# Performance work log

Measured on AMD Instinct MI355X. Metric: run time of the kernel, lower is better.

## Reference

```python
import jax, jax.numpy as jnp
import numpy as np

B, T, D, V, CD, NF = 2, 2048, 1024, 32000, 1024, 4
EPS_NORM = 1e-12
EPS_LN = 1e-5


def _gelu(x):
    return jax.nn.gelu(x, approximate=False)


def _l2norm(x):
    n = jnp.linalg.norm(x, axis=-1, keepdims=True)
    return x / jnp.maximum(n, EPS_NORM)


def setup_inputs() -> dict:
    key = jax.random.key(0)
    ks = jax.random.split(key, 24)
    s = 0.02
    inp = {
        "tokens": jax.random.randint(ks[0], (B, T), 0, V),
        "c_states": jax.random.normal(ks[1], (8, CD), dtype=jnp.float32),
        "embed": jax.random.normal(ks[2], (V, D), dtype=jnp.float32) * s,
        "pos_embed": jax.random.normal(ks[3], (T, D), dtype=jnp.float32) * s,
        # c_to_topo: Linear(c_dim,64) -> GELU -> Linear(64,2) -> Softplus (dead code in fwd, kept for completeness)
        "topo_W1": jax.random.normal(ks[4], (CD, 64), dtype=jnp.float32) * s,
        "topo_b1": jnp.zeros((64,), jnp.float32),
        "topo_W2": jax.random.normal(ks[5], (64, 2), dtype=jnp.float32) * s,
        "topo_b2": jnp.zeros((2,), jnp.float32),
        # c_to_thresh: Linear(c_dim,32) -> GELU -> Linear(32,NF) -> Sigmoid
        "thr_W1": jax.random.normal(ks[6], (CD, 32), dtype=jnp.float32) * s,
        "thr_b1": jnp.zeros((32,), jnp.float32),
        "thr_W2": jax.random.normal(ks[7], (32, NF), dtype=jnp.float32) * s,
        "thr_b2": jnp.zeros((NF,), jnp.float32),
        # simplex layers: NF x (Linear(2D,D) -> GELU -> Linear(D,D))
        "simp_W1": jax.random.normal(ks[8], (NF, 2 * D, D), dtype=jnp.float32) * s,
        "simp_b1": jnp.zeros((NF, D), jnp.float32),
        "simp_W2": jax.random.normal(ks[9], (NF, D, D), dtype=jnp.float32) * s,
        "simp_b2": jnp.zeros((NF, D), jnp.float32),
        # topo_integrate: Linear(D+2, 2D) -> GELU -> Linear(2D, D)
        "int_W1": jax.random.normal(ks[10], (D + 2, 2 * D), dtype=jnp.float32) * s,
        "int_b1": jnp.zeros((2 * D,), jnp.float32),
        "int_W2": jax.random.normal(ks[11], (2 * D, D), dtype=jnp.float32) * s,
        "int_b2": jnp.zeros((D,), jnp.float32),
        "ln_g": jnp.ones((D,), jnp.float32),
        "ln_b": jnp.zeros((D,), jnp.float32),
        "head_W": jax.random.normal(ks[12], (D, V), dtype=jnp.float32) * s,
    }
    return inp


def _forward(tokens, c_states, embed, pos_embed,
             topo_W1, topo_b1, topo_W2, topo_b2,
             thr_W1, thr_b1, thr_W2, thr_b2,
             simp_W1, simp_b1, simp_W2, simp_b2,
             int_W1, int_b1, int_W2, int_b2,
             ln_g, ln_b, head_W):
    b, t = tokens.shape
    x = embed[tokens] + pos_embed[jnp.arange(t)][None]          # [B,T,D]
    c_pooled = c_states.mean(axis=0)                            # [CD]
    thresholds = jax.nn.sigmoid(_gelu(c_pooled @ thr_W1 + thr_b1) @ thr_W2 + thr_b2)  # [NF]

    for level in range(NF):
        thresh = thresholds[level]
        x0 = x[0]                                               # [T,D] (module only uses batch elem 0)
        xn = _l2norm(x0)
        sim = xn @ xn.T                                         # [T,T]
        adj = jax.nn.sigmoid(10.0 * (sim - thresh))
        agg = adj @ x0                                          # dense message aggregation
        combined = jnp.concatenate([x0, agg], axis=-1)          # [T,2D]
        update = _gelu(combined @ simp_W1[level] + simp_b1[level]) @ simp_W2[level] + simp_b2[level]
        x = x + update[None] * 0.2                              # broadcast update across batch

    # approximate Betti numbers on detached embeddings
    xd = jax.lax.stop_gradient(x[0])
    xn = _l2norm(xd)
    sim = xn @ xn.T
    adj = jax.nn.sigmoid(10.0 * (sim - 0.5))
    degree = adj.sum(axis=-1)
    beta0 = (degree < 0.5).astype(jnp.float32).sum()
    n_edges = adj.sum() / 2.0
    beta1 = jax.nn.relu(n_edges - jnp.float32(t) + beta0 + 1.0)
    betti = jnp.stack([beta0, beta1])                           # [2]
    betti_exp = jnp.broadcast_to(betti[None, None, :], (b, t, 2))

    x = jnp.concatenate([x, betti_exp], axis=-1)                # [B,T,D+2]
    x = _gelu(x @ int_W1 + int_b1) @ int_W2 + int_b2            # [B,T,D]
    mu = x.mean(axis=-1, keepdims=True)
    var = x.var(axis=-1, keepdims=True)
    x = (x - mu) / jnp.sqrt(var + EPS_LN) * ln_g + ln_b
    return x @ head_W                                           # [B,T,V]


def reference(tokens, c_states, embed, pos_embed,
              topo_W1, topo_b1, topo_W2, topo_b2,
              thr_W1, thr_b1, thr_W2, thr_b2,
              simp_W1, simp_b1, simp_W2, simp_b2,
              int_W1, int_b1, int_W2, int_b2,
              ln_g, ln_b, head_W):
    return _forward(tokens, c_states, embed, pos_embed,
                    topo_W1, topo_b1, topo_W2, topo_b2,
                    thr_W1, thr_b1, thr_W2, thr_b2,
                    simp_W1, simp_b1, simp_W2, simp_b2,
                    int_W1, int_b1, int_W2, int_b2,
                    ln_g, ln_b, head_W)
```

## Files before the change

### kernel.cpp

```cpp
#include <hip/hip_runtime.h>

typedef __bf16 bf16;
using bf16x8 = __attribute__((ext_vector_type(8))) __bf16;
using bf16x4 = __attribute__((ext_vector_type(4))) __bf16;
using f32x4  = __attribute__((ext_vector_type(4))) float;

#define DEV __device__ __forceinline__
#define SCHED_FENCE() __builtin_amdgcn_sched_barrier(0)

DEV float gelu_f(float x){ return 0.5f*x*(1.0f+erff(x*0.7071067811865475f)); }
DEV float sigm_f(float x){ return 1.0f/(1.0f+expf(-x)); }

DEV void gload16(const bf16* g, bf16* l){
    __builtin_amdgcn_global_load_lds(
        (const __attribute__((address_space(1))) void*)g,
        (__attribute__((address_space(3))) void*)l, 16, 0, 0);
}

enum { EPI_ADJ=0, EPI_BF16=1, EPI_GELU_BIAS=2, EPI_XUPD=3, EPI_BIAS_F32=4, EPI_F32=5 };

template<int BM,int BN,int WM,int WN,int MINW,int EPI>
__global__ __launch_bounds__(WM*WN*64, MINW)
void gemm_p(const bf16* __restrict__ A, const bf16* __restrict__ B,
            int M, int N, int K, void* __restrict__ Cout, int ldc,
            const float* __restrict__ bias, const float* __restrict__ scal, int sidx,
            float* __restrict__ xu0, float* __restrict__ xu1)
{
    constexpr int THREADS = WM*WN*64;
    constexpr int MR = BM/WM/16, NR = BN/WN/16;
    constexpr int ATILE = BM*64, BTILE = BN*64;
    constexpr int RR = THREADS/8;
    constexpr int VM = (BM+BN)/RR;
    __shared__ bf16 sm[2*(ATILE+BTILE)];

    const int nbm = M/BM, nbn = N/BN;
    const int nwg = nbm*nbn;
    int wg = blockIdx.x;
    wg = (wg&7)*(nwg>>3) + (wg>>3);
    const int by = wg % nbm, bx = wg / nbm;
    const int tid = threadIdx.x, lane = tid&63, wid = tid>>6;
    const int wm = wid / WN, wn = wid % WN;
    const int fr = lane&15, fq = lane>>4;

    const bf16* Ab = A + (long)(by*BM + (tid>>3))*K + (((tid&7) ^ ((tid>>3)&7))<<3);
    const bf16* Bb = B + (long)(bx*BN + (tid>>3))*K + (((tid&7) ^ ((tid>>3)&7))<<3);

    auto STAGE = [&](int tt, int cb){
        bf16* d = sm + cb*(ATILE+BTILE) + wid*512;
        const long ko = (long)tt*64;
#pragma unroll
        for (int g=0; g<BM/RR; ++g)
            gload16(Ab + (long)g*RR*K + ko, d + g*RR*64);
#pragma unroll
        for (int g=0; g<BN/RR; ++g)
            gload16(Bb + (long)g*RR*K + ko, d + ATILE + g*RR*64);
    };

    f32x4 acc[MR][NR] = {};
    const int nt = K >> 6;

    STAGE(0,0);
    STAGE(1,1);

    for (int t=0; t<nt; ++t){
        const bf16* bufA = sm + (t&1)*(ATILE+BTILE);
        const bf16* bufB = bufA + ATILE;
        if (t+1<nt){
            if constexpr (VM==6)      asm volatile("s_waitcnt vmcnt(6)" ::: "memory");
            else if constexpr (VM==8) asm volatile("s_waitcnt vmcnt(8)" ::: "memory");
            else                      asm volatile("s_waitcnt vmcnt(0)" ::: "memory");
        } else {
            asm volatile("s_waitcnt vmcnt(0)" ::: "memory");
        }
        __builtin_amdgcn_s_barrier();
        __builtin_amdgcn_sched_barrier(0);
#pragma unroll
        for (int ks=0; ks<2; ++ks){
            bf16x8 af[MR], bv[NR];
            const int ch = (((ks*4+fq) ^ (fr&7))<<3);
#pragma unroll
            for (int j=0;j<MR;++j)
                af[j] = *(const bf16x8*)&bufA[(wm*(MR*16) + j*16 + fr)*64 + ch];
#pragma unroll
            for (int j=0;j<NR;++j)
                bv[j] = *(const bf16x8*)&bufB[(wn*(NR*16) + j*16 + fr)*64 + ch];
            __builtin_amdgcn_s_setprio(1);
#pragma unroll
            for (int mi=0;mi<MR;++mi)
#pragma unroll
            for (int ni=0;ni<NR;++ni)
                acc[mi][ni] = __builtin_amdgcn_mfma_f32_16x16x32_bf16(
                    af[mi], bv[ni], acc[mi][ni], 0,0,0);
            __builtin_amdgcn_s_setprio(0);
        }
        asm volatile("s_waitcnt lgkmcnt(0)" ::: "memory");
        __builtin_amdgcn_s_barrier();
        if (t+2<nt) STAGE(t+2, t&1);
    }

    float thr = 0.f;
    if constexpr (EPI==EPI_ADJ) thr = scal[sidx];

#pragma unroll
    for (int mi=0;mi<MR;++mi){
#pragma unroll
        for (int ni=0;ni<NR;++ni){
            const int col = bx*BN + wn*(NR*16) + ni*16 + fr;
#pragma unroll
            for (int r=0;r<4;++r){
                const int row = by*BM + wm*(MR*16) + mi*16 + fq*4 + r;
                const float v = acc[mi][ni][r];
                const long ci = (long)row*ldc + col;
                if constexpr (EPI==EPI_ADJ)       ((bf16*)Cout)[ci] = (bf16)sigm_f(10.f*(v - thr));
                else if constexpr (EPI==EPI_BF16) ((bf16*)Cout)[ci] = (bf16)v;
                else if constexpr (EPI==EPI_GELU_BIAS) ((bf16*)Cout)[ci] = (bf16)gelu_f(v + bias[col]);
                else if constexpr (EPI==EPI_BIAS_F32)  ((float*)Cout)[ci] = v + bias[col];
                else if constexpr (EPI==EPI_F32)       ((float*)Cout)[ci] = v;
                else if constexpr (EPI==EPI_XUPD){
                    const float u = 0.2f*(v + bias[col]);
                    xu0[ci] += u;  xu1[ci] += u;
                }
            }
        }
    }
}

template<int EPI>
__global__ __launch_bounds__(512, 2)
void gemm8(const bf16* __restrict__ A, const bf16* __restrict__ B,
           int M, int N, int K, void* __restrict__ Cout, int ldc,
           const float* __restrict__ bias)
{
    __shared__ bf16 sm[65536];
    const int nbm = M>>8, nbn = N>>8;
    const int nwg = nbm*nbn;
    int wg = blockIdx.x;
    wg = (wg&7)*(nwg>>3) + (wg>>3);
    const int bx = wg % nbn, by = wg / nbn;
    const int tid = threadIdx.x, lane = tid&63, wid = tid>>6;
    const int wm = wid>>2, wn = wid&3;
    const int fr = lane&15, fq = lane>>4;

    const bf16* Ag = A + (long)(by*256 + (tid>>3))*K + (((tid&7) ^ ((tid>>3)&7))<<3);
    const bf16* Bg = B + (long)(bx*256 + (tid>>3))*K + (((tid&7) ^ ((tid>>3)&7))<<3);

    auto SA = [&](int tt, int h){
        bf16* d = sm + (tt&1)*32768 + wid*512;
        const long ko = (long)tt*64;
        gload16(Ag + (long)(h*64)*K + ko,       d + h*4096);
        gload16(Ag + (long)(128+h*64)*K + ko,   d + 8192 + h*4096);
    };
    auto SB = [&](int tt, int h){
        bf16* d = sm + (tt&1)*32768 + 16384 + wid*512;
        const long ko = (long)tt*64;
#pragma unroll
        for (int g=0; g<2; ++g)
            gload16(Bg + (long)(h*2+g)*64*K + ko, d + (h*2+g)*4096);
    };

    f32x4 acc[8][4] = {};
    bf16x8 aCur[8], b0[4], b1[4];
    const int nt = K >> 6;

    SA(0,0); SB(0,0); SA(0,1); SB(0,1);
    SA(1,0); SB(1,0); SA(1,1);
    SCHED_FENCE();

    for (int t=0; t<nt; ++t){
        const bf16* bufA = sm + (t&1)*32768;
        const bf16* bufB = bufA + 16384;

        auto LDA = [&](int mh){
#pragma unroll
            for (int ks=0;ks<2;++ks){
                const int ch = (((ks*4+fq) ^ (fr&7))<<3);
#pragma unroll
                for (int j=0;j<4;++j)
                    aCur[ks*4+j] = *(const bf16x8*)&bufA[(wm*128 + mh*64 + j*16 + fr)*64 + ch];
            }
        };
        auto LDB = [&](int nh, bf16x8* dst){
#pragma unroll
            for (int ks=0;ks<2;++ks){
                const int ch = (((ks*4+fq) ^ (fr&7))<<3);
#pragma unroll
                for (int j=0;j<2;++j)
                    dst[ks*2+j] = *(const bf16x8*)&bufB[(wn*64 + nh*32 + j*16 + fr)*64 + ch];
            }
        };
        auto QMFMA = [&](int mh, int nh, bf16x8* bArr){
            __builtin_amdgcn_s_setprio(1);
#pragma unroll
            for (int ks=0;ks<2;++ks)
#pragma unroll
            for (int j=0;j<4;++j)
#pragma unroll
            for (int jj=0;jj<2;++jj)
                acc[mh*4+j][nh*2+jj] = __builtin_amdgcn_mfma_f32_16x16x32_bf16(
                    aCur[ks*4+j], bArr[ks*2+jj], acc[mh*4+j][nh*2+jj], 0,0,0);
            __builtin_amdgcn_s_setprio(0);
            SCHED_FENCE();
        };

        if (t+1<nt) asm volatile("s_waitcnt vmcnt(6)" ::: "memory");
        else        asm volatile("s_waitcnt vmcnt(0)" ::: "memory");
        __builtin_amdgcn_s_barrier();
        SCHED_FENCE();
        if (t+1<nt) SB(t+1,1);
        SCHED_FENCE();
        LDA(0); LDB(0, b0);
        asm volatile("s_waitcnt lgkmcnt(0)" ::: "memory");
        SCHED_FENCE();
        QMFMA(0,0,b0);
        __builtin_amdgcn_s_barrier();
        SCHED_FENCE();
        if (t+2<nt) SA(t+2,0);
        SCHED_FENCE();
        LDB(1, b1);
        asm volatile("s_waitcnt lgkmcnt(0)" ::: "memory");
        SCHED_FENCE();
        QMFMA(0,1,b1);
        __builtin_amdgcn_s_barrier();
        SCHED_FENCE();
        if (t+2<nt) SB(t+2,0);
        SCHED_FENCE();
        LDA(1);
        asm volatile("s_waitcnt lgkmcnt(0)" ::: "memory");
        SCHED_FENCE();
        QMFMA(1,1,b1);
        __builtin_amdgcn_s_barrier();
        SCHED_FENCE();
        if (t+2<nt) SA(t+2,1);
        SCHED_FENCE();
        QMFMA(1,0,b0);
    }

#pragma unroll
    for (int mi=0;mi<8;++mi){
#pragma unroll
        for (int ni=0;ni<4;++ni){
            const int col = bx*256 + wn*64 + ni*16 + fr;
#pragma unroll
            for (int r=0;r<4;++r){
                const int row = by*256 + wm*128 + mi*16 + fq*4 + r;
                const float v = acc[mi][ni][r];
                const long ci = (long)row*ldc + col;
                if constexpr (EPI==EPI_F32)            ((float*)Cout)[ci] = v;
                else if constexpr (EPI==EPI_BIAS_F32)  ((float*)Cout)[ci] = v + bias[col];
                else                                   ((bf16*)Cout)[ci] = (bf16)v;
            }
        }
    }
}

__global__ void prep_kernel(const float* __restrict__ cs,
                            const float* __restrict__ W1, const float* __restrict__ b1,
                            const float* __restrict__ W2, const float* __restrict__ b2,
                            float* __restrict__ thrs)
{
    __shared__ float cp[1024];
    __shared__ float part[8][32];
    __shared__ float h[32];
    const int tid = threadIdx.x;
    for (int j = tid; j < 1024; j += 256){
        float s = 0.f;
#pragma unroll
        for (int r = 0; r < 8; r++) s += cs[r*1024 + j];
        cp[j] = s * 0.125f;
    }
    __syncthreads();
    const int t = tid & 31, g = tid >> 5;
    float p = 0.f;
    for (int j = g*128; j < g*128+128; j++) p += cp[j] * W1[j*32 + t];
    part[g][t] = p;
    __syncthreads();
    if (tid < 32){
        float s = b1[tid];
#pragma unroll
        for (int q=0;q<8;q++) s += part[q][tid];
        h[tid] = gelu_f(s);
    }
    __syncthreads();
    if (tid < 4){
        float z = b2[tid];
        for (int k=0;k<32;k++) z += h[k]*W2[k*4 + tid];
        thrs[tid] = sigm_f(z);
    }
    if (tid == 4) thrs[4] = 0.5f;
}

__global__ void embed_kernel(const int* __restrict__ tok, const float* __restrict__ emb,
                             const float* __restrict__ pos, float* __restrict__ x)
{
    const long i = (long)blockIdx.x*256 + threadIdx.x;
    const int  d4 = i & 255;
    const long bt = i >> 8;
    const int  t  = (int)(bt & 2047);
    const int  token = tok[bt];
    f32x4 e = *(const f32x4*)(emb + (long)token*1024 + d4*4);
    f32x4 p = *(const f32x4*)(pos + (long)t*1024 + d4*4);
    *(f32x4*)(x + i*4) = e + p;
}

__global__ void transpose_f2b(const float* __restrict__ in, int ldin, long istr,
                              bf16* __restrict__ out, int ldout, long ostr,
                              int R, int C)
{
    __shared__ float tile[32][33];
    const int nbx = C >> 5, nby = R >> 5;
    const int per = nbx*nby;
    const int l  = blockIdx.x / per;
    const int rm = blockIdx.x % per;
    const int bx = rm % nbx, by = rm / nbx;
    const float* inl = in + (long)l*istr;
    bf16* outl = out + (long)l*ostr;
    const int tx = threadIdx.x & 31, ty = threadIdx.x >> 5;
#pragma unroll
    for (int i=0;i<32;i+=8)
        tile[ty+i][tx] = inl[(long)(by*32+ty+i)*ldin + bx*32+tx];
    __syncthreads();
#pragma unroll
    for (int i=0;i<32;i+=8)
        outl[(long)(bx*32+ty+i)*ldout + by*32+tx] = (bf16)tile[tx][ty+i];
}

__global__ void rownorm_kernel(const float* __restrict__ x, bf16* __restrict__ xn,
                               bf16* __restrict__ x0b, int ld0)
{
    const long t = blockIdx.x; const int tid = threadIdx.x;
    f32x4 v = *(const f32x4*)(x + t*1024 + tid*4);
    float s = v.x*v.x + v.y*v.y + v.z*v.z + v.w*v.w;
#pragma unroll
    for (int o=32;o>0;o>>=1) s += __shfl_down(s, o);
    __shared__ float red[4];
    if ((tid&63)==0) red[tid>>6] = s;
    __syncthreads();
    const float tot = red[0]+red[1]+red[2]+red[3];
    const float inv = 1.0f / fmaxf(sqrtf(tot), 1e-12f);
    bf16x4 a, b;
    a[0]=(bf16)(v.x*inv); a[1]=(bf16)(v.y*inv); a[2]=(bf16)(v.z*inv); a[3]=(bf16)(v.w*inv);
    b[0]=(bf16)v.x; b[1]=(bf16)v.y; b[2]=(bf16)v.z; b[3]=(bf16)v.w;
    *(bf16x4*)(xn  + t*1024 + tid*4) = a;
    *(bf16x4*)(x0b + t*ld0  + tid*4) = b;
}

__global__ void degree_kernel(const bf16* __restrict__ adj, float* __restrict__ deg)
{
    const long t = blockIdx.x; const int tid = threadIdx.x;
    bf16x8 v = *(const bf16x8*)(adj + t*2048 + tid*8);
    float s = 0.f;
#pragma unroll
    for (int j=0;j<8;j++) s += (float)v[j];
#pragma unroll
    for (int o=32;o>0;o>>=1) s += __shfl_down(s, o);
    __shared__ float red[4];
    if ((tid&63)==0) red[tid>>6] = s;
    __syncthreads();
    if (tid==0) deg[t] = red[0]+red[1]+red[2]+red[3];
}

__global__ void betti_kernel(const float* __restrict__ deg, float* __restrict__ betti)
{
    const int tid = threadIdx.x;
    float s = 0.f, c = 0.f;
#pragma unroll
    for (int i=0;i<8;i++){
        const float d = deg[tid*8 + i];
        s += d;  c += (d < 0.5f) ? 1.f : 0.f;
    }
#pragma unroll
    for (int o=32;o>0;o>>=1){ s += __shfl_down(s,o); c += __shfl_down(c,o); }
    __shared__ float ss[4], cc[4];
    if ((tid&63)==0){ ss[tid>>6]=s; cc[tid>>6]=c; }
    __syncthreads();
    if (tid==0){
        const float S = ss[0]+ss[1]+ss[2]+ss[3];
        const float C = cc[0]+cc[1]+cc[2]+cc[3];
        const float ne = 0.5f*S;
        const float b1 = ne - 2048.f + C + 1.f;
        betti[0] = C;
        betti[1] = b1 > 0.f ? b1 : 0.f;
    }
}

__global__ void b1eff_kernel(const float* __restrict__ ib1, const float* __restrict__ iW1,
                             const float* __restrict__ betti, float* __restrict__ out)
{
    const int j = blockIdx.x*256 + threadIdx.x;
    out[j] = ib1[j] + betti[0]*iW1[(long)1024*2048 + j] + betti[1]*iW1[(long)1025*2048 + j];
}

__global__ void f2b_kernel(const float* __restrict__ in, bf16* __restrict__ out)
{
    const long i = (long)blockIdx.x*256 + threadIdx.x;
    f32x4 a = *(const f32x4*)(in + i*8);
    f32x4 c = *(const f32x4*)(in + i*8 + 4);
    bf16x8 o;
    o[0]=(bf16)a.x; o[1]=(bf16)a.y; o[2]=(bf16)a.z; o[3]=(bf16)a.w;
    o[4]=(bf16)c.x; o[5]=(bf16)c.y; o[6]=(bf16)c.z; o[7]=(bf16)c.w;
    *(bf16x8*)(out + i*8) = o;
}

__global__ void ln_kernel(const float* __restrict__ y, const float* __restrict__ g,
                          const float* __restrict__ b, bf16* __restrict__ out)
{
    const long t = blockIdx.x; const int tid = threadIdx.x;
    f32x4 v = *(const f32x4*)(y + t*1024 + tid*4);
    float s  = v.x+v.y+v.z+v.w;
    float s2 = v.x*v.x+v.y*v.y+v.z*v.z+v.w*v.w;
#pragma unroll
    for (int o=32;o>0;o>>=1){ s += __shfl_down(s,o); s2 += __shfl_down(s2,o); }
    __shared__ float ss[4], qq[4];
    if ((tid&63)==0){ ss[tid>>6]=s; qq[tid>>6]=s2; }
    __syncthreads();
    const float S = ss[0]+ss[1]+ss[2]+ss[3], Q = qq[0]+qq[1]+qq[2]+qq[3];
    const float mu  = S * (1.f/1024.f);
    const float var = Q * (1.f/1024.f) - mu*mu;
    const float inv = rsqrtf(var + 1e-5f);
    f32x4 gv = *(const f32x4*)(g + tid*4);
    f32x4 bv = *(const f32x4*)(b + tid*4);
    bf16x4 o;
    o[0] = (bf16)((v.x - mu)*inv*gv.x + bv.x);
    o[1] = (bf16)((v.y - mu)*inv*gv.y + bv.y);
    o[2] = (bf16)((v.z - mu)*inv*gv.z + bv.z);
    o[3] = (bf16)((v.w - mu)*inv*gv.w + bv.w);
    *(bf16x4*)(out + t*1024 + tid*4) = o;
}

extern "C" void kernel_launch(void* const* d_in, const int* in_sizes, int n_in,
                              void* d_out, int out_size, void* d_ws, size_t ws_size,
                              hipStream_t stream)
{
    const int*   tokens = (const int*)  d_in[0];
    const float* cstate = (const float*)d_in[1];
    const float* embedW = (const float*)d_in[2];
    const float* posW   = (const float*)d_in[3];
    const float* thrW1  = (const float*)d_in[8];
    const float* thrb1  = (const float*)d_in[9];
    const float* thrW2  = (const float*)d_in[10];
    const float* thrb2  = (const float*)d_in[11];
    const float* simpW1 = (const float*)d_in[12];
    const float* simpb1 = (const float*)d_in[13];
    const float* simpW2 = (const float*)d_in[14];
    const float* simpb2 = (const float*)d_in[15];
    const float* intW1  = (const float*)d_in[16];
    const float* intb1  = (const float*)d_in[17];
    const float* intW2  = (const float*)d_in[18];
    const float* intb2  = (const float*)d_in[19];
    const float* lng    = (const float*)d_in[20];
    const float* lnb    = (const float*)d_in[21];
    const float* headW  = (const float*)d_in[22];
    float* out = (float*)d_out;

    size_t off = 0;
    auto carve = [&](size_t bytes) -> void* {
        void* p = (char*)d_ws + off;
        off += (bytes + 255) & ~(size_t)255;
        return p;
    };
    float* x_f32   = (float*)carve(16777216);
    bf16*  xn      = (bf16*) carve(4194304);
    bf16*  x0T     = (bf16*) carve(4194304);
    bf16*  comb    = (bf16*) carve(8388608);
    bf16*  adj     = (bf16*) carve(8388608);
    bf16*  h1      = (bf16*) carve(4194304);
    bf16*  xb      = (bf16*) carve(8388608);
    bf16*  w1T     = (bf16*) carve(16777216);
    bf16*  w2T     = (bf16*) carve(8388608);
    bf16*  i1T     = (bf16*) carve(4194304);
    bf16*  i2T     = (bf16*) carve(4194304);
    bf16*  hT      = (bf16*) carve(65536000);
    float* degree  = (float*)carve(8192);
    float* b1eff   = (float*)carve(8192);
    float* thrs    = (float*)carve(64);
    float* betti   = (float*)carve(64);
    bf16*  h2  = comb;
    float* yv  = x_f32;
    bf16*  xln = xn;

    const dim3 blk(256);
    const dim3 blk512(512);

    prep_kernel<<<1, blk, 0, stream>>>(cstate, thrW1, thrb1, thrW2, thrb2, thrs);
    embed_kernel<<<4096, blk, 0, stream>>>(tokens, embedW, posW, x_f32);

    transpose_f2b<<<4*(1024/32)*(2048/32), blk, 0, stream>>>(
        simpW1, 1024, (long)2048*1024, w1T, 2048, (long)1024*2048, 2048, 1024);
    transpose_f2b<<<4*(1024/32)*(1024/32), blk, 0, stream>>>(
        simpW2, 1024, (long)1024*1024, w2T, 1024, (long)1024*1024, 1024, 1024);
    transpose_f2b<<<(2048/32)*(1024/32), blk, 0, stream>>>(
        intW1, 2048, 0, i1T, 1024, 0, 1024, 2048);
    transpose_f2b<<<(1024/32)*(2048/32), blk, 0, stream>>>(
        intW2, 1024, 0, i2T, 2048, 0, 2048, 1024);
    transpose_f2b<<<(32000/32)*(1024/32), blk, 0, stream>>>(
        headW, 32000, 0, hT, 1024, 0, 1024, 32000);

    for (int l=0;l<4;l++){
        rownorm_kernel<<<2048, blk, 0, stream>>>(x_f32, xn, comb, 2048);
        transpose_f2b<<<(1024/32)*(2048/32), blk, 0, stream>>>(
            x_f32, 1024, 0, x0T, 2048, 0, 2048, 1024);
        gemm_p<128,128,2,2,2,EPI_ADJ><<<16*16, blk, 0, stream>>>(
            xn, xn, 2048, 2048, 1024, adj, 2048, nullptr, thrs, l, nullptr, nullptr);
        gemm_p<64,128,2,2,3,EPI_BF16><<<32*8, blk, 0, stream>>>(
            adj, x0T, 2048, 1024, 2048, comb + 1024, 2048, nullptr, nullptr, 0, nullptr, nullptr);
        gemm_p<64,128,2,2,3,EPI_GELU_BIAS><<<32*8, blk, 0, stream>>>(
            comb, w1T + (long)l*1024*2048, 2048, 1024, 2048, h1, 1024,
            simpb1 + l*1024, nullptr, 0, nullptr, nullptr);
        gemm_p<64,128,2,2,3,EPI_XUPD><<<32*8, blk, 0, stream>>>(
            h1, w2T + (long)l*1024*1024, 2048, 1024, 1024, nullptr, 1024,
            simpb2 + l*1024, nullptr, 0, x_f32, x_f32 + (long)2048*1024);
    }

    rownorm_kernel<<<2048, blk, 0, stream>>>(x_f32, xn, comb, 2048);
    gemm_p<128,128,2,2,2,EPI_ADJ><<<16*16, blk, 0, stream>>>(
        xn, xn, 2048, 2048, 1024, adj, 2048, nullptr, thrs, 4, nullptr, nullptr);
    degree_kernel<<<2048, blk, 0, stream>>>(adj, degree);
    betti_kernel<<<1, blk, 0, stream>>>(degree, betti);
    b1eff_kernel<<<8, blk, 0, stream>>>(intb1, intW1, betti, b1eff);

    f2b_kernel<<<2048, blk, 0, stream>>>(x_f32, xb);
    gemm_p<128,128,2,2,2,EPI_GELU_BIAS><<<32*16, blk, 0, stream>>>(
        xb, i1T, 4096, 2048, 1024, h2, 2048, b1eff, nullptr, 0, nullptr, nullptr);
    gemm_p<128,128,2,2,2,EPI_BIAS_F32><<<32*8, blk, 0, stream>>>(
        h2, i2T, 4096, 1024, 2048, yv, 1024, intb2, nullptr, 0, nullptr, nullptr);
    ln_kernel<<<4096, blk, 0, stream>>>(yv, lng, lnb, xln);
    gemm8<EPI_F32><<<16*125, blk512, 0, stream>>>(
        xln, hT, 4096, 32000, 1024, out, 32000, nullptr);
}
```

Baseline: 862.1 us.

## Compute symmetric adjacency upper triangle only and mirror; fuse bf16 cast into update

The Gram-matrix adjacency GEMM now launches only upper-triangular 128x128 tiles (136 instead of 256) and a new mirror kernel copies them across the diagonal, relying on the adjacency being symmetric. The last simplex update epilogue writes a bf16 copy of x directly, which removes the separate f2b conversion kernel. The final rownorm also skips its unused bf16 copy. Together these halve adjacency GEMM work and save several memory passes, at the cost of an extra transpose-style pass over half of adj and a serial tile-index loop. The 136 triangular tiles may also fill the GPU less evenly than 256 did.

```diff
diff --git a/kernel.cpp b/kernel.cpp
--- a/kernel.cpp
+++ b/kernel.cpp
@@ -17,14 +17,14 @@
         (__attribute__((address_space(3))) void*)l, 16, 0, 0);
 }
 
-enum { EPI_ADJ=0, EPI_BF16=1, EPI_GELU_BIAS=2, EPI_XUPD=3, EPI_BIAS_F32=4, EPI_F32=5 };
-
-template<int BM,int BN,int WM,int WN,int MINW,int EPI>
+enum { EPI_ADJ=0, EPI_BF16=1, EPI_GELU_BIAS=2, EPI_XUPD=3, EPI_BIAS_F32=4, EPI_F32=5, EPI_XUPDB=6 };
+
+template<int BM,int BN,int WM,int WN,int MINW,int TRIU,int EPI>
 __global__ __launch_bounds__(WM*WN*64, MINW)
 void gemm_p(const bf16* __restrict__ A, const bf16* __restrict__ B,
             int M, int N, int K, void* __restrict__ Cout, int ldc,
             const float* __restrict__ bias, const float* __restrict__ scal, int sidx,
-            float* __restrict__ xu0, float* __restrict__ xu1)
+            float* __restrict__ xu0, float* __restrict__ xu1, bf16* __restrict__ xbp)
 {
     constexpr int THREADS = WM*WN*64;
     constexpr int MR = BM/WM/16, NR = BN/WN/16;
@@ -34,10 +34,17 @@
     __shared__ bf16 sm[2*(ATILE+BTILE)];
 
     const int nbm = M/BM, nbn = N/BN;
-    const int nwg = nbm*nbn;
+    const int nwg = TRIU ? (nbm*(nbm+1))/2 : nbm*nbn;
     int wg = blockIdx.x;
     wg = (wg&7)*(nwg>>3) + (wg>>3);
-    const int by = wg % nbm, bx = wg / nbm;
+    int by, bx;
+    if constexpr (TRIU){
+        int i = wg, r = 0;
+        while (i >= nbm - r){ i -= nbm - r; ++r; }
+        by = r; bx = r + i;
+    } else {
+        by = wg % nbm; bx = wg / nbm;
+    }
     const int tid = threadIdx.x, lane = tid&63, wid = tid>>6;
     const int wm = wid / WN, wn = wid % WN;
     const int fr = lane&15, fq = lane>>4;
@@ -120,9 +127,35 @@
                     const float u = 0.2f*(v + bias[col]);
                     xu0[ci] += u;  xu1[ci] += u;
                 }
+                else if constexpr (EPI==EPI_XUPDB){
+                    const float u = 0.2f*(v + bias[col]);
+                    const float n0 = xu0[ci] + u, n1 = xu1[ci] + u;
+                    xu0[ci] = n0;  xu1[ci] = n1;
+                    xbp[ci] = (bf16)n0;
+                    xbp[ci + (long)2048*1024] = (bf16)n1;
+                }
             }
         }
     }
+}
+
+__global__ void mirror_kernel(bf16* __restrict__ adj)
+{
+    const int b = blockIdx.x;
+    int t128 = b >> 4, sub = b & 15;
+    int i = t128, BY = 1;
+    while (i >= BY){ i -= BY; ++BY; }
+    const int BX = i;
+    const int r0 = BY*128 + (sub>>2)*32, c0 = BX*128 + (sub&3)*32;
+    __shared__ bf16 tile[32][33];
+    const int tx = threadIdx.x & 31, ty = threadIdx.x >> 5;
+#pragma unroll
+    for (int k=0;k<32;k+=8)
+        tile[ty+k][tx] = adj[(long)(c0+ty+k)*2048 + r0+tx];
+    __syncthreads();
+#pragma unroll
+    for (int k=0;k<32;k+=8)
+        adj[(long)(r0+ty+k)*2048 + c0+tx] = tile[tx][ty+k];
 }
 
 template<int EPI>
@@ -337,11 +370,14 @@
     __syncthreads();
     const float tot = red[0]+red[1]+red[2]+red[3];
     const float inv = 1.0f / fmaxf(sqrtf(tot), 1e-12f);
-    bf16x4 a, b;
+    bf16x4 a;
     a[0]=(bf16)(v.x*inv); a[1]=(bf16)(v.y*inv); a[2]=(bf16)(v.z*inv); a[3]=(bf16)(v.w*inv);
-    b[0]=(bf16)v.x; b[1]=(bf16)v.y; b[2]=(bf16)v.z; b[3]=(bf16)v.w;
-    *(bf16x4*)(xn  + t*1024 + tid*4) = a;
-    *(bf16x4*)(x0b + t*ld0  + tid*4) = b;
+    *(bf16x4*)(xn + t*1024 + tid*4) = a;
+    if (x0b){
+        bf16x4 b;
+        b[0]=(bf16)v.x; b[1]=(bf16)v.y; b[2]=(bf16)v.z; b[3]=(bf16)v.w;
+        *(bf16x4*)(x0b + t*ld0 + tid*4) = b;
+    }
 }
 
 __global__ void degree_kernel(const bf16* __restrict__ adj, float* __restrict__ deg)
@@ -388,17 +424,6 @@
 {
     const int j = blockIdx.x*256 + threadIdx.x;
     out[j] = ib1[j] + betti[0]*iW1[(long)1024*2048 + j] + betti[1]*iW1[(long)1025*2048 + j];
-}
-
-__global__ void f2b_kernel(const float* __restrict__ in, bf16* __restrict__ out)
-{
-    const long i = (long)blockIdx.x*256 + threadIdx.x;
-    f32x4 a = *(const f32x4*)(in + i*8);
-    f32x4 c = *(const f32x4*)(in + i*8 + 4);
-    bf16x8 o;
-    o[0]=(bf16)a.x; o[1]=(bf16)a.y; o[2]=(bf16)a.z; o[3]=(bf16)a.w;
-    o[4]=(bf16)c.x; o[5]=(bf16)c.y; o[6]=(bf16)c.z; o[7]=(bf16)c.w;
-    *(bf16x8*)(out + i*8) = o;
 }
 
 __global__ void ln_kernel(const float* __restrict__ y, const float* __restrict__ g,
@@ -499,30 +524,36 @@
         rownorm_kernel<<<2048, blk, 0, stream>>>(x_f32, xn, comb, 2048);
         transpose_f2b<<<(1024/32)*(2048/32), blk, 0, stream>>>(
             x_f32, 1024, 0, x0T, 2048, 0, 2048, 1024);
-        gemm_p<128,128,2,2,2,EPI_ADJ><<<16*16, blk, 0, stream>>>(
-            xn, xn, 2048, 2048, 1024, adj, 2048, nullptr, thrs, l, nullptr, nullptr);
-        gemm_p<64,128,2,2,3,EPI_BF16><<<32*8, blk, 0, stream>>>(
-            adj, x0T, 2048, 1024, 2048, comb + 1024, 2048, nullptr, nullptr, 0, nullptr, nullptr);
-        gemm_p<64,128,2,2,3,EPI_GELU_BIAS><<<32*8, blk, 0, stream>>>(
+        gemm_p<128,128,2,2,2,1,EPI_ADJ><<<136, blk, 0, stream>>>(
+            xn, xn, 2048, 2048, 1024, adj, 2048, nullptr, thrs, l, nullptr, nullptr, nullptr);
+        mirror_kernel<<<1920, blk, 0, stream>>>(adj);
+        gemm_p<64,128,2,2,3,0,EPI_BF16><<<32*8, blk, 0, stream>>>(
+            adj, x0T, 2048, 1024, 2048, comb + 1024, 2048, nullptr, nullptr, 0, nullptr, nullptr, nullptr);
+        gemm_p<64,128,2,2,3,0,EPI_GELU_BIAS><<<32*8, blk, 0, stream>>>(
             comb, w1T + (long)l*1024*2048, 2048, 1024, 2048, h1, 1024,
-            simpb1 + l*1024, nullptr, 0, nullptr, nullptr);
-        gemm_p<64,128,2,2,3,EPI_XUPD><<<32*8, blk, 0, stream>>>(
-            h1, w2T + (long)l*1024*1024, 2048, 1024, 1024, nullptr, 1024,
-            simpb2 + l*1024, nullptr, 0, x_f32, x_f32 + (long)2048*1024);
-    }
-
-    rownorm_kernel<<<2048, blk, 0, stream>>>(x_f32, xn, comb, 2048);
-    gemm_p<128,128,2,2,2,EPI_ADJ><<<16*16, blk, 0, stream>>>(
-        xn, xn, 2048, 2048, 1024, adj, 2048, nullptr, thrs, 4, nullptr, nullptr);
+            simpb1 + l*1024, nullptr, 0, nullptr, nullptr, nullptr);
+        if (l < 3)
+            gemm_p<64,128,2,2,3,0,EPI_XUPD><<<32*8, blk, 0, stream>>>(
+                h1, w2T + (long)l*1024*1024, 2048, 1024, 1024, nullptr, 1024,
+                simpb2 + l*1024, nullptr, 0, x_f32, x_f32 + (long)2048*1024, nullptr);
+        else
+            gemm_p<64,128,2,2,3,0,EPI_XUPDB><<<32*8, blk, 0, stream>>>(
+                h1, w2T + (long)l*1024*1024, 2048, 1024, 1024, nullptr, 1024,
+                simpb2 + l*1024, nullptr, 0, x_f32, x_f32 + (long)2048*1024, xb);
+    }
+
+    rownorm_kernel<<<2048, blk, 0, stream>>>(x_f32, xn, nullptr, 0);
+    gemm_p<128,128,2,2,2,1,EPI_ADJ><<<136, blk, 0, stream>>>(
+        xn, xn, 2048, 2048, 1024, adj, 2048, nullptr, thrs, 4, nullptr, nullptr, nullptr);
+    mirror_kernel<<<1920, blk, 0, stream>>>(adj);
     degree_kernel<<<2048, blk, 0, stream>>>(adj, degree);
     betti_kernel<<<1, blk, 0, stream>>>(degree, betti);
     b1eff_kernel<<<8, blk, 0, stream>>>(intb1, intW1, betti, b1eff);
 
-    f2b_kernel<<<2048, blk, 0, stream>>>(x_f32, xb);
-    gemm_p<128,128,2,2,2,EPI_GELU_BIAS><<<32*16, blk, 0, stream>>>(
-        xb, i1T, 4096, 2048, 1024, h2, 2048, b1eff, nullptr, 0, nullptr, nullptr);
-    gemm_p<128,128,2,2,2,EPI_BIAS_F32><<<32*8, blk, 0, stream>>>(
-        h2, i2T, 4096, 1024, 2048, yv, 1024, intb2, nullptr, 0, nullptr, nullptr);
+    gemm_p<128,128,2,2,2,0,EPI_GELU_BIAS><<<32*16, blk, 0, stream>>>(
+        xb, i1T, 4096, 2048, 1024, h2, 2048, b1eff, nullptr, 0, nullptr, nullptr, nullptr);
+    gemm_p<128,128,2,2,2,0,EPI_BIAS_F32><<<32*8, blk, 0, stream>>>(
+        h2, i2T, 4096, 1024, 2048, yv, 1024, intb2, nullptr, 0, nullptr, nullptr, nullptr);
     ln_kernel<<<4096, blk, 0, stream>>>(yv, lng, lnb, xln);
     gemm8<EPI_F32><<<16*125, blk512, 0, stream>>>(
         xln, hT, 4096, 32000, 1024, out, 32000, nullptr);
```

Measured after the change: 873.5 us. About the same (+1.3%).
